# Kernel optimization log

Hardware: AMD Instinct MI355X
Metric: run time of the kernel (lower is better)

The kernel has to match this reference:

```python
import jax, jax.numpy as jnp
import numpy as np


def setup_inputs() -> dict:
    key = jax.random.key(0)
    k1, k2, k3, k4 = jax.random.split(key, 4)
    N, F_in, F_out = 8192, 512, 256
    inp = jax.random.normal(k1, (N, F_in), dtype=jnp.float32)
    adj = jax.random.uniform(k2, (N, N), dtype=jnp.float32)
    stdv = 1.0 / np.sqrt(F_out)
    weight = jax.random.uniform(k3, (F_in, F_out), minval=-stdv, maxval=stdv, dtype=jnp.float32)
    b = jax.random.uniform(k4, (F_out,), minval=-stdv, maxval=stdv, dtype=jnp.float32)
    return {"input": inp, "adj": adj, "weight": weight, "b": b}


def reference(input, adj, weight, b):
    N = adj.shape[0]
    degree = jnp.sum(adj, axis=1)                      # [N]
    # A_tilde = 2*I - adj
    A_tilde = 2.0 * jnp.eye(N, dtype=adj.dtype) - adj
    d_inv_sqrt = 1.0 / jnp.sqrt(2.0 + degree)          # [N]
    # D^-1/2 @ A_tilde @ D^-1/2 as broadcasted row/col scaling (same math, O(N^2))
    L_sharpen = d_inv_sqrt[:, None] * A_tilde * d_inv_sqrt[None, :]
    support = input @ weight                           # [N, F_out]
    out = L_sharpen @ support + b                      # [N, F_out]
    return jax.nn.relu(out)
```

## Files before the change

kernel.cpp:

```cpp
#include <hip/hip_runtime.h>


typedef _Float16 h4 __attribute__((ext_vector_type(4)));
typedef _Float16 h8 __attribute__((ext_vector_type(8)));
typedef float f4 __attribute__((ext_vector_type(4)));

__device__ __forceinline__ void gload_lds16(const void* g, void* l) {
    __builtin_amdgcn_global_load_lds(
        (const __attribute__((address_space(1))) void*)g,
        (__attribute__((address_space(3))) void*)l, 16, 0, 0);
}

__device__ __forceinline__ void gload2(const float* p, f4& x, f4& y) {
    asm volatile("global_load_dwordx4 %0, %2, off\n\t"
                 "global_load_dwordx4 %1, %2, off offset:16"
                 : "=&v"(x), "=&v"(y)
                 : "v"(p)
                 : "memory");
}
__device__ __forceinline__ void gloadBfrag(const char* p, h8& x, h8& y) {
    asm volatile("global_load_dwordx4 %0, %2, off\n\t"
                 "global_load_dwordx4 %1, %2, off offset:1024"
                 : "=&v"(x), "=&v"(y)
                 : "v"(p)
                 : "memory");
}

__global__ __launch_bounds__(256) void k0_wt(const float* __restrict__ weight,
                                             char* __restrict__ wt) {
    const int idx = blockIdx.x * 256 + threadIdx.x;
    const int k = idx >> 8, j = idx & 255;
    const _Float16 h = (_Float16)weight[idx];
    const int off = j * 1024 + ((k >> 6) << 7) + (((k & 63) << 1) ^ ((j & 7) << 4));
    *(_Float16*)(wt + off) = h;
}

__global__ __launch_bounds__(256) void k1_deg(const float* __restrict__ adj,
                                              float* __restrict__ dinv) {
    const int r = blockIdx.x;
    const float4* rp = (const float4*)(adj + (size_t)r * 8192);
    const int t = threadIdx.x;
    float s = 0.f;
#pragma unroll
    for (int i = 0; i < 8; ++i) {
        float4 v = rp[t + i * 256];
        s += (v.x + v.y) + (v.z + v.w);
    }
#pragma unroll
    for (int off = 32; off > 0; off >>= 1) s += __shfl_down(s, off, 64);
    __shared__ float part[4];
    if ((t & 63) == 0) part[t >> 6] = s;
    __syncthreads();
    if (t == 0) {
        float deg = (part[0] + part[1]) + (part[2] + part[3]);
        dinv[r] = 1.0f / sqrtf(2.0f + deg);
    }
}

__global__ __launch_bounds__(512) void k2_support(const float* __restrict__ input,
                                                  const char* __restrict__ wt,
                                                  const float* __restrict__ dinv,
                                                  char* __restrict__ sT) {
    __shared__ char smem[4096 + 32768];
    const int t = threadIdx.x, w = t >> 6, l = t & 63;
    const int r0 = (int)blockIdx.x * 32;
    const int arow = t >> 4, ak4 = t & 15;
    const int bj = l >> 3, bb = (l & 7) * 16;

    f4 acc[2][2] = {};

    for (int kt = 0; kt < 8; ++kt) {
        const int k0 = kt * 64;
        __syncthreads();
        {
            float4 v = *(const float4*)(input + (size_t)(r0 + arow) * 512 + k0 + ak4 * 4);
            h4 h;
            h[0] = (_Float16)v.x; h[1] = (_Float16)v.y;
            h[2] = (_Float16)v.z; h[3] = (_Float16)v.w;
            *(h4*)(smem + arow * 128 + ((ak4 * 8) ^ ((arow & 7) << 4))) = h;
        }
#pragma unroll
        for (int q = 0; q < 4; ++q) {
            const int c = q * 8 + w;
            gload_lds16(wt + (size_t)(c * 8 + bj) * 1024 + kt * 128 + bb,
                        smem + 4096 + c * 1024);
        }
        __syncthreads();
#pragma unroll
        for (int kk = 0; kk < 2; ++kk) {
            const int ko = kk * 64 + ((l >> 4) << 4);
            h8 a[2], b[2];
#pragma unroll
            for (int m = 0; m < 2; ++m) {
                const int r = m * 16 + (l & 15);
                a[m] = *(const h8*)(smem + r * 128 + (ko ^ ((r & 7) << 4)));
            }
#pragma unroll
            for (int n = 0; n < 2; ++n) {
                const int j = w * 32 + n * 16 + (l & 15);
                b[n] = *(const h8*)(smem + 4096 + j * 128 + (ko ^ ((j & 7) << 4)));
            }
#pragma unroll
            for (int m = 0; m < 2; ++m)
#pragma unroll
                for (int n = 0; n < 2; ++n)
                    acc[m][n] = __builtin_amdgcn_mfma_f32_16x16x32_f16(a[m], b[n], acc[m][n], 0, 0, 0);
        }
    }
#pragma unroll
    for (int m = 0; m < 2; ++m)
#pragma unroll
        for (int n = 0; n < 2; ++n) {
            const int j = w * 32 + n * 16 + (l & 15);
            const int k0r = r0 + m * 16 + ((l >> 4) << 2);
            h4 h;
#pragma unroll
            for (int r = 0; r < 4; ++r)
                h[r] = (_Float16)(dinv[k0r + r] * acc[m][n][r]);
            const int off = (((j >> 4) * 128 + (k0r >> 6)) << 11) +
                            (((k0r >> 5) & 1) << 10) +
                            ((((k0r >> 3) & 3) << 4) + (j & 15)) * 16 +
                            ((k0r & 7) << 1);
            *(h4*)(sT + off) = h;
        }
}

__global__ __launch_bounds__(512, 4) void k3_spmm(const float* __restrict__ adj,
                                                  const char* __restrict__ sT,
                                                  float* __restrict__ part,
                                                  float* __restrict__ out,
                                                  int steps) {
    __shared__ __align__(16) char smem[2][32768];
    const int t = threadIdx.x;
    const int w = t >> 6, l = t & 63;
    const int i0 = (int)blockIdx.x * 64;
    const int ks0 = (int)blockIdx.y * steps * 256;
    const int ts_d = ((unsigned)(i0 - ks0) < (unsigned)(steps * 256))
                     ? ((i0 - ks0) >> 8) : -1;

    const int arow = t >> 3;
    const int ak16 = (t & 7) * 16;
    const int arow_g = i0 + arow;
    const float* aptr = adj + (size_t)arow_g * 8192 + ks0 + ak16;
    const int aswz = (arow & 7) << 4;
    const int abase = arow * 512;

    const char* bpn0 = sT + ((size_t)(w * 2) * 128 + (ks0 >> 6)) * 2048 + l * 16;
    const char* bpn1 = bpn0 + 262144;

    f4 acc[4][2] = {};
    h8 bvA[2][2], bvB[2][2];
    f4 pa0, pa1, pa2, pa3;
    f4 pb0, pb1, pb2, pb3;

    auto loadB = [&](int s, h8 (&bv)[2][2]) {
        gloadBfrag(bpn0 + (size_t)s * 2048, bv[0][0], bv[1][0]);
        gloadBfrag(bpn1 + (size_t)s * 2048, bv[0][1], bv[1][1]);
    };
    auto loadAr = [&](int tile, int r, f4& x0, f4& y0, f4& x1, f4& y1) {
        const float* p = aptr + (size_t)tile * 256 + r * 128;
        gload2(p, x0, y0);
        gload2(p + 8, x1, y1);
    };
    auto writeAr = [&](char* buf, int tile, int r,
                       const f4 x0, const f4 y0, const f4 x1, const f4 y1) {
        h8 u, v;
        if (tile == ts_d) {
            const int kg = ks0 + tile * 256 + ak16 + r * 128;
#pragma unroll
            for (int e = 0; e < 4; ++e) {
                u[e]     = (_Float16)((arow_g == kg + e     ) ? 2.0f - x0[e] : -x0[e]);
                u[4 + e] = (_Float16)((arow_g == kg + 4 + e ) ? 2.0f - y0[e] : -y0[e]);
                v[e]     = (_Float16)((arow_g == kg + 8 + e ) ? 2.0f - x1[e] : -x1[e]);
                v[4 + e] = (_Float16)((arow_g == kg + 12 + e) ? 2.0f - y1[e] : -y1[e]);
            }
        } else {
#pragma unroll
            for (int e = 0; e < 4; ++e) {
                u[e] = (_Float16)(-x0[e]); u[4 + e] = (_Float16)(-y0[e]);
                v[e] = (_Float16)(-x1[e]); v[4 + e] = (_Float16)(-y1[e]);
            }
        }
        const int kb = (ak16 << 1) + r * 256;
        *(h8*)(buf + abase + (kb ^ aswz)) = u;
        *(h8*)(buf + abase + ((kb + 16) ^ aswz)) = v;
    };
    auto compute = [&](const char* A, int sp, const h8 (&bv)[2][2]) {
#pragma unroll
        for (int kk = 0; kk < 2; ++kk) {
            const int kb = sp * 128 + kk * 64 + ((l >> 4) << 4);
            h8 a[4];
#pragma unroll
            for (int m = 0; m < 4; ++m) {
                const int r = m * 16 + (l & 15);
                a[m] = *(const h8*)(A + r * 512 + (kb ^ ((r & 7) << 4)));
            }
#pragma unroll
            for (int m = 0; m < 4; ++m)
#pragma unroll
                for (int n = 0; n < 2; ++n)
                    acc[m][n] = __builtin_amdgcn_mfma_f32_16x16x32_f16(a[m], bv[kk][n], acc[m][n], 0, 0, 0);
        }
    };

#define SBAR0() __builtin_amdgcn_sched_barrier(0)
#define WAIT_BV(N, BV)                                                        \
    asm volatile("s_waitcnt vmcnt(" #N ")"                                    \
                 : "+v"(BV[0][0]), "+v"(BV[0][1]),                            \
                   "+v"(BV[1][0]), "+v"(BV[1][1]) :: "memory");               \
    SBAR0();
#define WAIT_BVA(N, BV, X0, Y0, X1, Y1)                                       \
    asm volatile("s_waitcnt vmcnt(" #N ")"                                    \
                 : "+v"(BV[0][0]), "+v"(BV[0][1]),                            \
                   "+v"(BV[1][0]), "+v"(BV[1][1]),                            \
                   "+v"(X0), "+v"(Y0), "+v"(X1), "+v"(Y1) :: "memory");       \
    SBAR0();
#define BARRIER()                                                             \
    asm volatile("s_waitcnt lgkmcnt(0)\n\ts_barrier" ::: "memory");           \
    SBAR0();

    loadAr(0, 0, pa0, pa1, pa2, pa3);
    loadAr(0, 1, pb0, pb1, pb2, pb3);
    loadB(0, bvA);
    asm volatile("s_waitcnt vmcnt(8)"
                 : "+v"(pa0), "+v"(pa1), "+v"(pa2), "+v"(pa3) :: "memory");
    SBAR0();
    writeAr(smem[0], 0, 0, pa0, pa1, pa2, pa3);
    asm volatile("s_waitcnt vmcnt(4)"
                 : "+v"(pb0), "+v"(pb1), "+v"(pb2), "+v"(pb3) :: "memory");
    SBAR0();
    writeAr(smem[0], 0, 1, pb0, pb1, pb2, pb3);
    BARRIER()

    for (int ts = 0; ts + 1 < steps; ++ts) {
        char* AC = smem[ts & 1];
        char* AN = smem[(ts & 1) ^ 1];
        const int s0 = ts * 4;
        loadB(s0 + 1, bvB);
        WAIT_BV(4, bvA)
        compute(AC, 0, bvA);

        loadB(s0 + 2, bvA);
        loadAr(ts + 1, 0, pa0, pa1, pa2, pa3);
        WAIT_BV(8, bvB)
        compute(AC, 1, bvB);

        loadB(s0 + 3, bvB);
        WAIT_BVA(4, bvA, pa0, pa1, pa2, pa3)
        writeAr(AN, ts + 1, 0, pa0, pa1, pa2, pa3);
        loadAr(ts + 1, 1, pb0, pb1, pb2, pb3);
        compute(AC, 2, bvA);

        loadB(s0 + 4, bvA);
        WAIT_BVA(4, bvB, pb0, pb1, pb2, pb3)
        writeAr(AN, ts + 1, 1, pb0, pb1, pb2, pb3);
        compute(AC, 3, bvB);
        BARRIER()
    }
    {
        const char* AC = smem[(steps - 1) & 1];
        const int s0 = (steps - 1) * 4;
        loadB(s0 + 1, bvB);
        WAIT_BV(4, bvA)
        compute(AC, 0, bvA);
        loadB(s0 + 2, bvA);
        WAIT_BV(4, bvB)
        compute(AC, 1, bvB);
        loadB(s0 + 3, bvB);
        WAIT_BV(4, bvA)
        compute(AC, 2, bvA);
        WAIT_BV(0, bvB)
        compute(AC, 3, bvB);
    }
#undef SBAR0
#undef WAIT_BV
#undef WAIT_BVA
#undef BARRIER

    float* dst = (blockIdx.y == gridDim.y - 1) ? out
               : part + (size_t)blockIdx.y * (8192 * 256);
#pragma unroll
    for (int m = 0; m < 4; ++m)
#pragma unroll
        for (int n = 0; n < 2; ++n) {
            const int j = w * 32 + n * 16 + (l & 15);
            const int ib = i0 + m * 16 + ((l >> 4) << 2);
#pragma unroll
            for (int r = 0; r < 4; ++r)
                dst[(size_t)(ib + r) * 256 + j] = acc[m][n][r];
        }
}

__global__ __launch_bounds__(256) void k4_fin(const float* __restrict__ part,
                                              float* __restrict__ out,
                                              const float* __restrict__ dinv,
                                              const float* __restrict__ bias,
                                              int nsplit) {
    const int idx = blockIdx.x * 256 + threadIdx.x;
    float4 s = ((const float4*)out)[idx];
    for (int sp = 0; sp < nsplit - 1; ++sp)
        s += ((const float4*)(part + (size_t)sp * (8192 * 256)))[idx];
    const float dv = dinv[idx >> 6];
    const float4 b = ((const float4*)bias)[idx & 63];
    float4 r;
    r.x = fmaxf(dv * s.x + b.x, 0.f);
    r.y = fmaxf(dv * s.y + b.y, 0.f);
    r.z = fmaxf(dv * s.z + b.z, 0.f);
    r.w = fmaxf(dv * s.w + b.w, 0.f);
    ((float4*)out)[idx] = r;
}

extern "C" void kernel_launch(void* const* d_in, const int* in_sizes, int n_in,
                              void* d_out, int out_size, void* d_ws, size_t ws_size,
                              hipStream_t stream) {
    const float* input  = (const float*)d_in[0];
    const float* adj    = (const float*)d_in[1];
    const float* weight = (const float*)d_in[2];
    const float* bias   = (const float*)d_in[3];
    float* out = (float*)d_out;

    char* ws = (char*)d_ws;
    float* dinv = (float*)ws;
    char*  wt   = ws + 32768;
    char*  sT   = ws + 294912;
    float* part = (float*)(ws + 294912 + 4194304);

    const size_t base = 294912 + 4194304;
    int nsplit = 1;
    if (ws_size >= base + 3 * 8388608) nsplit = 4;
    else if (ws_size >= base + 1 * 8388608) nsplit = 2;
    const int steps = 8192 / (nsplit * 256);

    k0_wt<<<512, 256, 0, stream>>>(weight, wt);
    k1_deg<<<8192, 256, 0, stream>>>(adj, dinv);
    k2_support<<<256, 512, 0, stream>>>(input, wt, dinv, sT);
    k3_spmm<<<dim3(128, nsplit), 512, 0, stream>>>(adj, sT, part, out, steps);
    k4_fin<<<2048, 256, 0, stream>>>(part, out, dinv, bias, nsplit);
}
```

Baseline: 138.4 us.

## Convert adjacency to swizzled fp16 during degree pass, stream it into SpMM

```diff
diff --git a/kernel.cpp b/kernel.cpp
--- a/kernel.cpp
+++ b/kernel.cpp
@@ -36,15 +36,33 @@
 }
 
 __global__ __launch_bounds__(256) void k1_deg(const float* __restrict__ adj,
-                                              float* __restrict__ dinv) {
+                                              float* __restrict__ dinv,
+                                              char* __restrict__ adjH,
+                                              int do_h) {
     const int r = blockIdx.x;
     const float4* rp = (const float4*)(adj + (size_t)r * 8192);
     const int t = threadIdx.x;
+    const int swz = (r & 7) << 4;
     float s = 0.f;
 #pragma unroll
-    for (int i = 0; i < 8; ++i) {
-        float4 v = rp[t + i * 256];
-        s += (v.x + v.y) + (v.z + v.w);
+    for (int i = 0; i < 4; ++i) {
+        const float4 v0 = rp[t * 2 + i * 512];
+        const float4 v1 = rp[t * 2 + 1 + i * 512];
+        s += ((v0.x + v0.y) + (v0.z + v0.w)) + ((v1.x + v1.y) + (v1.z + v1.w));
+        if (do_h) {
+            const int k = t * 8 + i * 2048;
+            h8 h;
+            h[0] = (_Float16)((r == k    ) ? 2.0f - v0.x : -v0.x);
+            h[1] = (_Float16)((r == k + 1) ? 2.0f - v0.y : -v0.y);
+            h[2] = (_Float16)((r == k + 2) ? 2.0f - v0.z : -v0.z);
+            h[3] = (_Float16)((r == k + 3) ? 2.0f - v0.w : -v0.w);
+            h[4] = (_Float16)((r == k + 4) ? 2.0f - v1.x : -v1.x);
+            h[5] = (_Float16)((r == k + 5) ? 2.0f - v1.y : -v1.y);
+            h[6] = (_Float16)((r == k + 6) ? 2.0f - v1.z : -v1.z);
+            h[7] = (_Float16)((r == k + 7) ? 2.0f - v1.w : -v1.w);
+            const int off = ((k >> 6) << 7) + (((k & 63) << 1) ^ swz);
+            *(h8*)(adjH + (size_t)r * 16384 + off) = h;
+        }
     }
 #pragma unroll
     for (int off = 32; off > 0; off >>= 1) s += __shfl_down(s, off, 64);
@@ -125,11 +143,112 @@
         }
 }
 
-__global__ __launch_bounds__(512, 4) void k3_spmm(const float* __restrict__ adj,
+__global__ __launch_bounds__(512, 4) void k3_spmm(const char* __restrict__ adjH,
                                                   const char* __restrict__ sT,
                                                   float* __restrict__ part,
                                                   float* __restrict__ out,
                                                   int steps) {
+    __shared__ __align__(16) char smem[2][8192];
+    const int t = threadIdx.x;
+    const int w = t >> 6, l = t & 63;
+    const int i0 = (int)blockIdx.x * 64;
+    const int ks0 = (int)blockIdx.y * steps * 64;
+
+    const char* asrc = adjH + (size_t)(i0 + (t >> 3)) * 16384 +
+                       ((size_t)(ks0 >> 6) << 7) + ((t & 7) << 4);
+    const char* bpn0 = sT + ((size_t)(w * 2) * 128 + (ks0 >> 6)) * 2048 + l * 16;
+    const char* bpn1 = bpn0 + 262144;
+
+    f4 acc[4][2] = {};
+    h8 bvA[2][2], bvB[2][2];
+
+    auto stageA = [&](int kt, int buf) {
+        gload_lds16(asrc + (size_t)kt * 128, smem[buf] + w * 1024);
+    };
+    auto loadB = [&](int kt, h8 (&bv)[2][2]) {
+        gloadBfrag(bpn0 + (size_t)kt * 2048, bv[0][0], bv[1][0]);
+        gloadBfrag(bpn1 + (size_t)kt * 2048, bv[0][1], bv[1][1]);
+    };
+    auto compute = [&](const char* A, const h8 (&bv)[2][2]) {
+#pragma unroll
+        for (int kk = 0; kk < 2; ++kk) {
+            const int ko = kk * 64 + ((l >> 4) << 4);
+            h8 a[4];
+#pragma unroll
+            for (int m = 0; m < 4; ++m) {
+                const int r = m * 16 + (l & 15);
+                a[m] = *(const h8*)(A + r * 128 + (ko ^ ((r & 7) << 4)));
+            }
+#pragma unroll
+            for (int m = 0; m < 4; ++m)
+#pragma unroll
+                for (int n = 0; n < 2; ++n)
+                    acc[m][n] = __builtin_amdgcn_mfma_f32_16x16x32_f16(a[m], bv[kk][n], acc[m][n], 0, 0, 0);
+        }
+    };
+
+#define SBAR0() __builtin_amdgcn_sched_barrier(0)
+#define WAIT_BV(N, BV)                                                        \
+    asm volatile("s_waitcnt vmcnt(" #N ")"                                    \
+                 : "+v"(BV[0][0]), "+v"(BV[0][1]),                            \
+                   "+v"(BV[1][0]), "+v"(BV[1][1]) :: "memory");               \
+    SBAR0();
+#define WAIT_VM(N)                                                            \
+    asm volatile("s_waitcnt vmcnt(" #N ")" ::: "memory");                     \
+    SBAR0();
+#define BARRIER4()                                                            \
+    asm volatile("s_waitcnt vmcnt(4) lgkmcnt(0)\n\ts_barrier" ::: "memory");  \
+    SBAR0();
+
+    stageA(0, 0);
+    loadB(0, bvA);
+    WAIT_VM(4)
+    asm volatile("s_waitcnt lgkmcnt(0)\n\ts_barrier" ::: "memory");
+    SBAR0();
+
+#define BODY(kt, BVC, BVN, CUR)                                               \
+    {                                                                         \
+        stageA((kt) + 1, (CUR) ^ 1);                                          \
+        loadB((kt) + 1, BVN);                                                 \
+        WAIT_BV(5, BVC)                                                       \
+        compute(smem[CUR], BVC);                                              \
+        BARRIER4()                                                            \
+    }
+
+    for (int kt2 = 0; kt2 + 2 < steps; kt2 += 2) {
+        BODY(kt2,     bvA, bvB, 0)
+        BODY(kt2 + 1, bvB, bvA, 1)
+    }
+    BODY(steps - 2, bvA, bvB, 0)
+    {
+        WAIT_BV(0, bvB)
+        compute(smem[1], bvB);
+    }
+#undef BODY
+#undef WAIT_BV
+#undef WAIT_VM
+#undef BARRIER4
+#undef SBAR0
+
+    float* dst = (blockIdx.y == gridDim.y - 1) ? out
+               : part + (size_t)blockIdx.y * (8192 * 256);
+#pragma unroll
+    for (int m = 0; m < 4; ++m)
+#pragma unroll
+        for (int n = 0; n < 2; ++n) {
+            const int j = w * 32 + n * 16 + (l & 15);
+            const int ib = i0 + m * 16 + ((l >> 4) << 2);
+#pragma unroll
+            for (int r = 0; r < 4; ++r)
+                dst[(size_t)(ib + r) * 256 + j] = acc[m][n][r];
+        }
+}
+
+__global__ __launch_bounds__(512, 4) void k3_f32(const float* __restrict__ adj,
+                                                 const char* __restrict__ sT,
+                                                 float* __restrict__ part,
+                                                 float* __restrict__ out,
+                                                 int steps) {
     __shared__ __align__(16) char smem[2][32768];
     const int t = threadIdx.x;
     const int w = t >> 6, l = t & 63;
@@ -150,8 +269,7 @@
 
     f4 acc[4][2] = {};
     h8 bvA[2][2], bvB[2][2];
-    f4 pa0, pa1, pa2, pa3;
-    f4 pb0, pb1, pb2, pb3;
+    f4 pa0, pa1, pa2, pa3, pb0, pb1, pb2, pb3;
 
     auto loadB = [&](int s, h8 (&bv)[2][2]) {
         gloadBfrag(bpn0 + (size_t)s * 2048, bv[0][0], bv[1][0]);
@@ -324,16 +442,24 @@
     char*  wt   = ws + 32768;
     char*  sT   = ws + 294912;
     float* part = (float*)(ws + 294912 + 4194304);
+    char*  adjH = ws + 33554432;
 
     const size_t base = 294912 + 4194304;
+    const size_t need_h = 33554432ull + 134217728ull;
     int nsplit = 1;
     if (ws_size >= base + 3 * 8388608) nsplit = 4;
     else if (ws_size >= base + 1 * 8388608) nsplit = 2;
-    const int steps = 8192 / (nsplit * 256);
+    const bool use_h = (ws_size >= need_h) && (nsplit == 4);
 
     k0_wt<<<512, 256, 0, stream>>>(weight, wt);
-    k1_deg<<<8192, 256, 0, stream>>>(adj, dinv);
+    k1_deg<<<8192, 256, 0, stream>>>(adj, dinv, adjH, use_h ? 1 : 0);
     k2_support<<<256, 512, 0, stream>>>(input, wt, dinv, sT);
-    k3_spmm<<<dim3(128, nsplit), 512, 0, stream>>>(adj, sT, part, out, steps);
+    if (use_h) {
+        const int steps = 8192 / (nsplit * 64);
+        k3_spmm<<<dim3(128, nsplit), 512, 0, stream>>>(adjH, sT, part, out, steps);
+    } else {
+        const int steps = 8192 / (nsplit * 256);
+        k3_f32<<<dim3(128, nsplit), 512, 0, stream>>>(adj, sT, part, out, steps);
+    }
     k4_fin<<<2048, 256, 0, stream>>>(part, out, dinv, bias, nsplit);
 }
```

Result: slower. 164.9 us (+19.2%).
